# Optimization experiments

Hardware: AMD Instinct MI355X
Metric: run time of the kernel (lower is better)

Reference implementation:

```python
import jax, jax.numpy as jnp
import numpy as np
from jax import lax

B, C, H, W = 8, 512, 64, 64
HM, WM = 256, 256
EPS = 1e-08


def _nearest_downsample(mask, H_out, W_out):
    # torch F.interpolate(mode='nearest'): src_idx = floor(dst_idx * in/out)
    h_in, w_in = mask.shape[-2:]
    ri = (jnp.arange(H_out) * h_in) // H_out
    ci = (jnp.arange(W_out) * w_in) // W_out
    return mask[:, :, ri][:, :, :, ci]


def _dilate3x3(m):
    # binary dilation with 3x3 ones structuring element == 3x3 max-pool, zero pad
    return lax.reduce_window(m, 0.0, lax.max, (1, 1, 3, 3), (1, 1, 1, 1),
                             [(0, 0), (0, 0), (1, 1), (1, 1)])


def _edt(mask2d):
    # Exact Euclidean distance from each pixel to nearest mask==1 pixel.
    # mask2d: [B, H, W] float 0/1. Separable two-pass squared EDT.
    b, h, w = mask2d.shape
    BIG = jnp.asarray(h + w, mask2d.dtype)
    rows = jnp.arange(h)
    di = jnp.abs(rows[:, None] - rows[None, :]).astype(mask2d.dtype)  # [H, H']
    # g[b,i,j] = min_{i'} |i - i'| s.t. mask[b,i',j]==1 (BIG if column empty)
    g = jnp.min(di[None, :, :, None] + BIG * (1.0 - mask2d)[:, None, :, :], axis=2)  # [B,H,W]
    cols = jnp.arange(w)
    dj2 = ((cols[:, None] - cols[None, :]) ** 2).astype(mask2d.dtype)  # [W, W']
    d2 = jnp.min(g[:, :, None, :] ** 2 + dj2[None, None, :, :], axis=3)  # [B,H,W]
    dist = jnp.sqrt(d2)
    dist = dist / (jnp.max(dist, axis=(1, 2), keepdims=True) + 1e-06)
    return dist


def setup_inputs() -> dict:
    key = jax.random.key(0)
    k1, k2, k3, k4, k5 = jax.random.split(key, 5)
    f_s = jax.random.normal(k1, (B, C, H, W), dtype=jnp.float32)
    support_mask = jax.random.randint(k2, (B, 1, HM, WM), 0, 2, dtype=jnp.int32)
    sg = 1.0 / np.sqrt(C)
    gate_w = jax.random.uniform(k3, (C, C), jnp.float32, -sg, sg)
    gate_b = jnp.zeros((C,), jnp.float32)
    sf = 1.0 / np.sqrt(C + 1)
    fusion_w = jax.random.uniform(k4, (C, C + 1), jnp.float32, -sf, sf)
    fusion_b = jnp.zeros((C,), jnp.float32)
    return {"f_s": f_s, "support_mask": support_mask, "gate_w": gate_w,
            "gate_b": gate_b, "fusion_w": fusion_w, "fusion_b": fusion_b}


def reference(f_s, support_mask, gate_w, gate_b, fusion_w, fusion_b):
    m_s = _nearest_downsample(support_mask, f_s.shape[2], f_s.shape[3]).astype(f_s.dtype)  # [B,1,H,W]
    m_dil = _dilate3x3(m_s)
    m_bg = jnp.clip(m_dil - m_s, 0.0, None)

    p_fg = jnp.sum(f_s * m_s, axis=(2, 3)) / (jnp.sum(m_s, axis=(2, 3)) + EPS)   # [B,C]
    p_bg = jnp.sum(f_s * m_bg, axis=(2, 3)) / (jnp.sum(m_bg, axis=(2, 3)) + EPS)  # [B,C]
    p_contrast = (p_fg - p_bg)[:, :, None, None]

    gate = jax.nn.sigmoid(jnp.einsum('bchw,oc->bohw', f_s, gate_w) + gate_b[None, :, None, None])
    f_pur = f_s + gate * p_contrast

    dist = _edt(m_s[:, 0])[:, None]  # [B,1,H,W]
    x = jnp.concatenate([f_pur, dist], axis=1)  # [B,C+1,H,W]
    out = jnp.einsum('bchw,oc->bohw', x, fusion_w) + fusion_b[None, :, None, None]
    return jax.nn.relu(out)
```

## Files before the change

### kernel.cpp

```cpp
#include <hip/hip_runtime.h>
#include <math.h>

#define NB 8
#define CC 512
#define NPIX 4096
#define HM 256

#define WS_MS    0
#define WS_MBG   32768
#define WS_DIST  65536
#define WS_CNT   98304
#define WS_PC    98320
#define WS_GWP   102416
#define WS_FWP   364560
#define WS_FSPK  626704
#define WS_FPPK  17403920

typedef __attribute__((ext_vector_type(8))) short short8;
typedef __attribute__((ext_vector_type(4))) float f32x4;

__device__ __forceinline__ uint32_t packbf(float x) {
    uint32_t b = __float_as_uint(x);
    uint32_t hi = (b + 0x7fffu + ((b >> 16) & 1u)) & 0xffff0000u;
    float rem = x - __uint_as_float(hi);
    uint32_t rb = __float_as_uint(rem);
    uint32_t lo = (rb + 0x7fffu + ((rb >> 16) & 1u)) >> 16;
    return hi | lo;
}
__device__ __forceinline__ float unpackf(uint32_t u) {
    return __uint_as_float(u & 0xffff0000u) + __uint_as_float(u << 16);
}

__device__ __forceinline__ float wave_sum(float v) {
#pragma unroll
    for (int o = 32; o > 0; o >>= 1) v += __shfl_down(v, o, 64);
    return v;
}
__device__ __forceinline__ float wave_max(float v) {
#pragma unroll
    for (int o = 32; o > 0; o >>= 1) v = fmaxf(v, __shfl_down(v, o, 64));
    return v;
}

__global__ __launch_bounds__(1024) void mask_edt_kernel(
    const int* __restrict__ mask, float* __restrict__ ms, float* __restrict__ mbg,
    float* __restrict__ dist, float* __restrict__ cnt)
{
    __shared__ float sm[4096];
    __shared__ float sg[4096];
    __shared__ float red[32];

    const int b = blockIdx.x;
    const int t = threadIdx.x;
    const int wid = t >> 6, lane = t & 63;
    const int* mb = mask + b * (HM * HM);

#pragma unroll
    for (int u = 0; u < 4; ++u) {
        int p = u * 1024 + t;
        int i = p >> 6, j = p & 63;
        sm[p] = (float)mb[(i * 4) * HM + (j * 4)];
    }
    __syncthreads();

    float cfg = 0.f, cbg = 0.f;
#pragma unroll
    for (int u = 0; u < 4; ++u) {
        int p = u * 1024 + t;
        int i = p >> 6, j = p & 63;
        float mx = 0.f;
#pragma unroll
        for (int di = -1; di <= 1; ++di) {
            int ii = i + di;
            if (ii < 0 || ii > 63) continue;
#pragma unroll
            for (int dj = -1; dj <= 1; ++dj) {
                int jj = j + dj;
                if (jj < 0 || jj > 63) continue;
                mx = fmaxf(mx, sm[ii * 64 + jj]);
            }
        }
        float m = sm[p];
        float bg = fmaxf(mx - m, 0.f);
        cfg += m; cbg += bg;
        ms[b * NPIX + p] = m;
        mbg[b * NPIX + p] = bg;
    }
    float s1 = wave_sum(cfg), s2 = wave_sum(cbg);
    if (lane == 0) { red[wid] = s1; red[16 + wid] = s2; }
    __syncthreads();
    if (t == 0) {
        float a = 0.f, g = 0.f;
#pragma unroll
        for (int w = 0; w < 16; ++w) { a += red[w]; g += red[16 + w]; }
        cnt[b] = a; cnt[8 + b] = g;
    }

#pragma unroll 1
    for (int u = 0; u < 4; ++u) {
        int p = u * 1024 + t;
        int i = p >> 6, j = p & 63;
        float fi = (float)i;
        float best = 1e30f;
#pragma unroll 8
        for (int ii = 0; ii < 64; ++ii) {
            float v = fabsf(fi - (float)ii) + 128.f * (1.f - sm[ii * 64 + j]);
            best = fminf(best, v);
        }
        sg[p] = best;
    }
    __syncthreads();

    float dmx = 0.f;
#pragma unroll 1
    for (int u = 0; u < 4; ++u) {
        int p = u * 1024 + t;
        int i = p >> 6, j = p & 63;
        float fj = (float)j;
        float best = 1e30f;
#pragma unroll 8
        for (int jj = 0; jj < 64; ++jj) {
            float g = sg[i * 64 + jj];
            float dj = fj - (float)jj;
            best = fminf(best, fmaf(g, g, dj * dj));
        }
        float d = sqrtf(best);
        sm[p] = d;
        dmx = fmaxf(dmx, d);
    }
    __syncthreads();
    float mW = wave_max(dmx);
    if (lane == 0) red[wid] = mW;
    __syncthreads();
    float dmax = red[0];
#pragma unroll
    for (int w = 1; w < 16; ++w) dmax = fmaxf(dmax, red[w]);
    dmax += 1e-6f;
#pragma unroll
    for (int u = 0; u < 4; ++u) {
        int p = u * 1024 + t;
        dist[b * NPIX + p] = sm[p] / dmax;
    }
}

__global__ __launch_bounds__(256) void pcontrast_kernel(
    const float* __restrict__ F, const float* __restrict__ ms,
    const float* __restrict__ mbg, const float* __restrict__ cnt,
    float* __restrict__ pc)
{
    const int c = blockIdx.x, b = blockIdx.y, t = threadIdx.x;
    const float4* f4 = (const float4*)(F + ((size_t)b * CC + c) * NPIX);
    const float4* m4 = (const float4*)(ms + (size_t)b * NPIX);
    const float4* g4 = (const float4*)(mbg + (size_t)b * NPIX);
    float sfg = 0.f, sbg = 0.f;
#pragma unroll 4
    for (int idx = t; idx < NPIX / 4; idx += 256) {
        float4 v = f4[idx], m = m4[idx], g = g4[idx];
        sfg += v.x * m.x + v.y * m.y + v.z * m.z + v.w * m.w;
        sbg += v.x * g.x + v.y * g.y + v.z * g.z + v.w * g.w;
    }
    __shared__ float r1[4], r2[4];
    sfg = wave_sum(sfg); sbg = wave_sum(sbg);
    int wid = t >> 6, lane = t & 63;
    if (lane == 0) { r1[wid] = sfg; r2[wid] = sbg; }
    __syncthreads();
    if (t == 0) {
        float a = r1[0] + r1[1] + r1[2] + r1[3];
        float g = r2[0] + r2[1] + r2[2] + r2[3];
        pc[b * CC + c] = a / (cnt[b] + 1e-8f) - g / (cnt[8 + b] + 1e-8f);
    }
}

__global__ __launch_bounds__(256) void transpose_pack(
    const float* __restrict__ F, uint32_t* __restrict__ Fp)
{
    __shared__ float sm[64][65];
    const int b  = blockIdx.z;
    const int c0 = blockIdx.y * 64;
    const int p0 = blockIdx.x * 64;
    const int t  = threadIdx.x;
    const float* Fb = F + ((size_t)b * CC + c0) * NPIX + p0;
#pragma unroll
    for (int s = 0; s < 4; ++s) {
        int cl = s * 16 + (t >> 4);
        float4 v = *(const float4*)&Fb[(size_t)cl * NPIX + (t & 15) * 4];
        *(float4*)&sm[cl][(t & 15) * 4] = v;
    }
    __syncthreads();
    const int lane = t & 63, w = t >> 6;
    uint32_t* Op = Fp + ((size_t)b * NPIX + p0) * CC + c0;
#pragma unroll
    for (int s = 0; s < 16; ++s) {
        int pl = s * 4 + w;
        Op[(size_t)pl * CC + lane] = packbf(sm[lane][pl]);
    }
}

__global__ __launch_bounds__(256) void pack_weights(
    const float* __restrict__ gw, const float* __restrict__ fw,
    uint32_t* __restrict__ gwp, uint32_t* __restrict__ fwp)
{
    const int o = blockIdx.x, t = threadIdx.x;
#pragma unroll 2
    for (int c = t; c < CC; c += 256) {
        gwp[o * CC + c] = packbf(gw[o * CC + c]);
        fwp[o * CC + c] = packbf(fw[o * (CC + 1) + c]);
    }
}

#define STAGE_TILE(dA, dB, ktU)                                                          \
    do {                                                                                 \
        _Pragma("unroll")                                                                \
        for (int r_ = 0; r_ < 4; ++r_) {                                                 \
            int grp_ = r_ * 4 + wid;                                                     \
            int row_ = grp_ * 8 + l8;                                                    \
            const uint32_t* gA_ = Ab + (size_t)(mBase + row_) * CC + (ktU) + k16src * 4; \
            const uint32_t* gB_ = Bb + (size_t)(nBase + row_) * CC + (ktU) + k16src * 4; \
            __builtin_amdgcn_global_load_lds(                                            \
                (const __attribute__((address_space(1))) uint32_t*)gA_,                  \
                (__attribute__((address_space(3))) uint32_t*)&dA[grp_ * 256 + lane * 4], \
                16, 0, 0);                                                               \
            __builtin_amdgcn_global_load_lds(                                            \
                (const __attribute__((address_space(1))) uint32_t*)gB_,                  \
                (__attribute__((address_space(3))) uint32_t*)&dB[grp_ * 256 + lane * 4], \
                16, 0, 0);                                                               \
        }                                                                                \
    } while (0)

#define COMPUTE_TILE(sA, sB)                                                             \
    do {                                                                                 \
        short8 hA_[4], lA_[4];                                                           \
        _Pragma("unroll")                                                                \
        for (int fm_ = 0; fm_ < 4; ++fm_) {                                              \
            int row_ = wr * 64 + fm_ * 16 + fr;                                          \
            int base_ = row_ * 32, s_ = row_ & 7;                                        \
            uint4 x0_ = *(const uint4*)&sA[base_ + (((kc * 2)     ^ s_) << 2)];          \
            uint4 x1_ = *(const uint4*)&sA[base_ + (((kc * 2 + 1) ^ s_) << 2)];          \
            uint32_t pk_[8] = {x0_.x, x0_.y, x0_.z, x0_.w, x1_.x, x1_.y, x1_.z, x1_.w};  \
            _Pragma("unroll")                                                            \
            for (int j_ = 0; j_ < 8; ++j_) {                                             \
                hA_[fm_][j_] = (short)(pk_[j_] >> 16);                                   \
                lA_[fm_][j_] = (short)(pk_[j_] & 0xffffu);                               \
            }                                                                            \
        }                                                                                \
        _Pragma("unroll")                                                                \
        for (int fn_ = 0; fn_ < 4; ++fn_) {                                              \
            int row_ = wc * 64 + fn_ * 16 + fr;                                          \
            int base_ = row_ * 32, s_ = row_ & 7;                                        \
            uint4 x0_ = *(const uint4*)&sB[base_ + (((kc * 2)     ^ s_) << 2)];          \
            uint4 x1_ = *(const uint4*)&sB[base_ + (((kc * 2 + 1) ^ s_) << 2)];          \
            uint32_t pk_[8] = {x0_.x, x0_.y, x0_.z, x0_.w, x1_.x, x1_.y, x1_.z, x1_.w};  \
            short8 hB_, lB_;                                                             \
            _Pragma("unroll")                                                            \
            for (int j_ = 0; j_ < 8; ++j_) {                                             \
                hB_[j_] = (short)(pk_[j_] >> 16);                                        \
                lB_[j_] = (short)(pk_[j_] & 0xffffu);                                    \
            }                                                                            \
            _Pragma("unroll")                                                            \
            for (int fm_ = 0; fm_ < 4; ++fm_) {                                          \
                acc[fm_][fn_] = __builtin_amdgcn_mfma_f32_16x16x32_bf16(hA_[fm_], hB_, acc[fm_][fn_], 0, 0, 0); \
                acc[fm_][fn_] = __builtin_amdgcn_mfma_f32_16x16x32_bf16(hA_[fm_], lB_, acc[fm_][fn_], 0, 0, 0); \
                acc[fm_][fn_] = __builtin_amdgcn_mfma_f32_16x16x32_bf16(lA_[fm_], hB_, acc[fm_][fn_], 0, 0, 0); \
            }                                                                            \
        }                                                                                \
    } while (0)

template <int MODE>
__global__ __launch_bounds__(256, 2) void mfma_gemm(
    const uint32_t* __restrict__ Apk, const uint32_t* __restrict__ Bpk,
    long aStride, long bStride,
    const float* __restrict__ bias,
    const float* __restrict__ aux,
    const float* __restrict__ wsrc,
    void* __restrict__ outp)
{
    const int gx = gridDim.x, gy = gridDim.y;
    const int nwg = gx * gy * gridDim.z;
    int lin = (blockIdx.z * gy + blockIdx.y) * gx + blockIdx.x;
    int cpx = nwg >> 3;
    int swz = (lin & 7) * cpx + (lin >> 3);
    const int bx = swz % gx;
    const int by = (swz / gx) % gy;
    const int b  = swz / (gx * gy);

    const int nBase = bx * 128;
    const int mBase = by * 128;
    const int tid   = threadIdx.x;
    const int lane  = tid & 63, wid = tid >> 6;
    const int wr    = wid >> 1, wc = wid & 1;

    __shared__ uint32_t As0[128 * 32];
    __shared__ uint32_t Bs0[128 * 32];
    __shared__ uint32_t As1[128 * 32];
    __shared__ uint32_t Bs1[128 * 32];

    const uint32_t* Ab = Apk + (size_t)b * aStride;
    const uint32_t* Bb = Bpk + (size_t)b * bStride;

    f32x4 acc[4][4];
#pragma unroll
    for (int i = 0; i < 4; ++i)
#pragma unroll
        for (int j = 0; j < 4; ++j) acc[i][j] = (f32x4){0.f, 0.f, 0.f, 0.f};

    const int l8 = lane >> 3;
    const int k16src = (lane & 7) ^ l8;
    const int fr = lane & 15;
    const int kc = lane >> 4;

    STAGE_TILE(As0, Bs0, 0);
    __syncthreads();

#pragma unroll 1
    for (int it2 = 0; it2 < 8; ++it2) {
        const int ktU1 = it2 * 64 + 32;
        STAGE_TILE(As1, Bs1, ktU1);
        COMPUTE_TILE(As0, Bs0);
        __syncthreads();
        if (it2 < 7) {
            STAGE_TILE(As0, Bs0, ktU1 + 32);
        }
        COMPUTE_TILE(As1, Bs1);
        __syncthreads();
    }

    const int rrow = (lane >> 4) * 4;
    if constexpr (MODE == 0) {
        uint32_t* fpur = (uint32_t*)outp;
#pragma unroll
        for (int fn = 0; fn < 4; ++fn) {
            int o = nBase + wc * 64 + fn * 16 + fr;
            float bo  = bias[o];
            float pco = aux[(size_t)b * CC + o];
#pragma unroll
            for (int fm = 0; fm < 4; ++fm) {
#pragma unroll
                for (int r = 0; r < 4; ++r) {
                    int p = mBase + wr * 64 + fm * 16 + rrow + r;
                    size_t idx = (size_t)p * CC + o;
                    float fs = unpackf(Ab[idx]);
                    float z = acc[fm][fn][r] + bo;
                    float g = 1.f / (1.f + expf(-z));
                    fpur[(size_t)b * NPIX * CC + idx] = packbf(fs + g * pco);
                }
            }
        }
    } else {
        float* Out = (float*)outp;
#pragma unroll
        for (int fn = 0; fn < 4; ++fn) {
            int p = nBase + wc * 64 + fn * 16 + fr;
            float dv = aux[(size_t)b * NPIX + p];
#pragma unroll
            for (int fm = 0; fm < 4; ++fm) {
#pragma unroll
                for (int r = 0; r < 4; ++r) {
                    int o = mBase + wr * 64 + fm * 16 + rrow + r;
                    float z = acc[fm][fn][r] + bias[o] + wsrc[(size_t)o * (CC + 1) + CC] * dv;
                    Out[((size_t)b * CC + o) * NPIX + p] = fmaxf(z, 0.f);
                }
            }
        }
    }
}

extern "C" void kernel_launch(void* const* d_in, const int* in_sizes, int n_in,
                              void* d_out, int out_size, void* d_ws, size_t ws_size,
                              hipStream_t stream)
{
    const float* f_s      = (const float*)d_in[0];
    const int*   mask     = (const int*)d_in[1];
    const float* gate_w   = (const float*)d_in[2];
    const float* gate_b   = (const float*)d_in[3];
    const float* fusion_w = (const float*)d_in[4];
    const float* fusion_b = (const float*)d_in[5];
    float* out = (float*)d_out;
    float*    wsf = (float*)d_ws;
    uint32_t* wsu = (uint32_t*)d_ws;

    float* ms   = wsf + WS_MS;
    float* mbg  = wsf + WS_MBG;
    float* dist = wsf + WS_DIST;
    float* cnt  = wsf + WS_CNT;
    float* pc   = wsf + WS_PC;
    uint32_t* gwp  = wsu + WS_GWP;
    uint32_t* fwp  = wsu + WS_FWP;
    uint32_t* fspk = wsu + WS_FSPK;
    uint32_t* fppk = wsu + WS_FPPK;

    hipLaunchKernelGGL(mask_edt_kernel, dim3(NB), dim3(1024), 0, stream,
                       mask, ms, mbg, dist, cnt);
    hipLaunchKernelGGL(pack_weights, dim3(CC), dim3(256), 0, stream,
                       gate_w, fusion_w, gwp, fwp);
    hipLaunchKernelGGL(transpose_pack, dim3(NPIX / 64, CC / 64, NB), dim3(256), 0, stream,
                       f_s, fspk);
    hipLaunchKernelGGL(pcontrast_kernel, dim3(CC, NB), dim3(256), 0, stream,
                       f_s, ms, mbg, cnt, pc);
    hipLaunchKernelGGL((mfma_gemm<0>), dim3(CC / 128, NPIX / 128, NB), dim3(256), 0, stream,
                       fspk, gwp, (long)NPIX * CC, 0L, gate_b, pc, (const float*)nullptr,
                       (void*)fppk);
    hipLaunchKernelGGL((mfma_gemm<1>), dim3(NPIX / 128, CC / 128, NB), dim3(256), 0, stream,
                       fwp, fppk, 0L, (long)NPIX * CC, fusion_b, dist, fusion_w,
                       (void*)out);
}
```

Measured before the change: 344.5 us.

## Store split-bf16 operands as separate hi and lo planes instead of packed words

Each fp32 value is still split into a high and a low bf16 half. These halves are now written by the pack, transpose and gate-GEMM epilogue kernels into two separate ushort arrays instead of one packed uint32 array. The GEMM stages four planes into LDS and loads short8 fragments directly, removing the per-element shift and mask unpacking before each MFMA. In exchange it drops the XOR swizzle, which may cause LDS bank conflicts. It also doubles the number of narrower 2-byte scattered loads and stores in the epilogue.

```diff
diff --git a/kernel.cpp b/kernel.cpp
--- a/kernel.cpp
+++ b/kernel.cpp
@@ -11,10 +11,14 @@
 #define WS_DIST  65536
 #define WS_CNT   98304
 #define WS_PC    98320
-#define WS_GWP   102416
-#define WS_FWP   364560
-#define WS_FSPK  626704
-#define WS_FPPK  17403920
+#define WS_GWH   102416
+#define WS_GWL   233488
+#define WS_FWH   364560
+#define WS_FWL   495632
+#define WS_FSH   626704
+#define WS_FSL   9015312
+#define WS_FPH   17403920
+#define WS_FPL   25792528
 
 typedef __attribute__((ext_vector_type(8))) short short8;
 typedef __attribute__((ext_vector_type(4))) float f32x4;
@@ -27,8 +31,8 @@
     uint32_t lo = (rb + 0x7fffu + ((rb >> 16) & 1u)) >> 16;
     return hi | lo;
 }
-__device__ __forceinline__ float unpackf(uint32_t u) {
-    return __uint_as_float(u & 0xffff0000u) + __uint_as_float(u << 16);
+__device__ __forceinline__ float joinbf(uint32_t h, uint32_t l) {
+    return __uint_as_float(h << 16) + __uint_as_float(l << 16);
 }
 
 __device__ __forceinline__ float wave_sum(float v) {
@@ -172,7 +176,7 @@
 }
 
 __global__ __launch_bounds__(256) void transpose_pack(
-    const float* __restrict__ F, uint32_t* __restrict__ Fp)
+    const float* __restrict__ F, ushort* __restrict__ Fh, ushort* __restrict__ Fl)
 {
     __shared__ float sm[64][65];
     const int b  = blockIdx.z;
@@ -188,74 +192,67 @@
     }
     __syncthreads();
     const int lane = t & 63, w = t >> 6;
-    uint32_t* Op = Fp + ((size_t)b * NPIX + p0) * CC + c0;
+    size_t ob = ((size_t)b * NPIX + p0) * CC + c0;
 #pragma unroll
     for (int s = 0; s < 16; ++s) {
         int pl = s * 4 + w;
-        Op[(size_t)pl * CC + lane] = packbf(sm[lane][pl]);
+        uint32_t u = packbf(sm[lane][pl]);
+        Fh[ob + (size_t)pl * CC + lane] = (ushort)(u >> 16);
+        Fl[ob + (size_t)pl * CC + lane] = (ushort)(u & 0xffffu);
     }
 }
 
 __global__ __launch_bounds__(256) void pack_weights(
     const float* __restrict__ gw, const float* __restrict__ fw,
-    uint32_t* __restrict__ gwp, uint32_t* __restrict__ fwp)
+    ushort* __restrict__ gwh, ushort* __restrict__ gwl,
+    ushort* __restrict__ fwh, ushort* __restrict__ fwl)
 {
     const int o = blockIdx.x, t = threadIdx.x;
 #pragma unroll 2
     for (int c = t; c < CC; c += 256) {
-        gwp[o * CC + c] = packbf(gw[o * CC + c]);
-        fwp[o * CC + c] = packbf(fw[o * (CC + 1) + c]);
-    }
-}
-
-#define STAGE_TILE(dA, dB, ktU)                                                          \
+        uint32_t ug = packbf(gw[o * CC + c]);
+        uint32_t uf = packbf(fw[o * (CC + 1) + c]);
+        gwh[o * CC + c] = (ushort)(ug >> 16); gwl[o * CC + c] = (ushort)(ug & 0xffffu);
+        fwh[o * CC + c] = (ushort)(uf >> 16); fwl[o * CC + c] = (ushort)(uf & 0xffffu);
+    }
+}
+
+#define STAGE_PLANE(dst, gsrc)                                                           \
     do {                                                                                 \
         _Pragma("unroll")                                                                \
-        for (int r_ = 0; r_ < 4; ++r_) {                                                 \
-            int grp_ = r_ * 4 + wid;                                                     \
-            int row_ = grp_ * 8 + l8;                                                    \
-            const uint32_t* gA_ = Ab + (size_t)(mBase + row_) * CC + (ktU) + k16src * 4; \
-            const uint32_t* gB_ = Bb + (size_t)(nBase + row_) * CC + (ktU) + k16src * 4; \
+        for (int c_ = 0; c_ < 2; ++c_) {                                                 \
+            int grp_ = c_ * 4 + wid;                                                     \
+            const ushort* s_ = (gsrc) + (size_t)(grp_ * 16 + (lane >> 2)) * CC           \
+                               + (lane & 3) * 8;                                         \
             __builtin_amdgcn_global_load_lds(                                            \
-                (const __attribute__((address_space(1))) uint32_t*)gA_,                  \
-                (__attribute__((address_space(3))) uint32_t*)&dA[grp_ * 256 + lane * 4], \
-                16, 0, 0);                                                               \
-            __builtin_amdgcn_global_load_lds(                                            \
-                (const __attribute__((address_space(1))) uint32_t*)gB_,                  \
-                (__attribute__((address_space(3))) uint32_t*)&dB[grp_ * 256 + lane * 4], \
+                (const __attribute__((address_space(1))) uint32_t*)s_,                   \
+                (__attribute__((address_space(3))) uint32_t*)&dst[grp_ * 256 + lane * 4],\
                 16, 0, 0);                                                               \
         }                                                                                \
     } while (0)
 
-#define COMPUTE_TILE(sA, sB)                                                             \
+#define STAGE_TILE(dAh, dAl, dBh, dBl, ktE)                                              \
+    do {                                                                                 \
+        STAGE_PLANE(dAh, Abh + (size_t)mBase * CC + (ktE));                              \
+        STAGE_PLANE(dAl, Abl + (size_t)mBase * CC + (ktE));                              \
+        STAGE_PLANE(dBh, Bbh + (size_t)nBase * CC + (ktE));                              \
+        STAGE_PLANE(dBl, Bbl + (size_t)nBase * CC + (ktE));                              \
+    } while (0)
+
+#define COMPUTE_TILE(sAh, sAl, sBh, sBl)                                                 \
     do {                                                                                 \
         short8 hA_[4], lA_[4];                                                           \
         _Pragma("unroll")                                                                \
         for (int fm_ = 0; fm_ < 4; ++fm_) {                                              \
-            int row_ = wr * 64 + fm_ * 16 + fr;                                          \
-            int base_ = row_ * 32, s_ = row_ & 7;                                        \
-            uint4 x0_ = *(const uint4*)&sA[base_ + (((kc * 2)     ^ s_) << 2)];          \
-            uint4 x1_ = *(const uint4*)&sA[base_ + (((kc * 2 + 1) ^ s_) << 2)];          \
-            uint32_t pk_[8] = {x0_.x, x0_.y, x0_.z, x0_.w, x1_.x, x1_.y, x1_.z, x1_.w};  \
-            _Pragma("unroll")                                                            \
-            for (int j_ = 0; j_ < 8; ++j_) {                                             \
-                hA_[fm_][j_] = (short)(pk_[j_] >> 16);                                   \
-                lA_[fm_][j_] = (short)(pk_[j_] & 0xffffu);                               \
-            }                                                                            \
+            int ro_ = (wr * 64 + fm_ * 16 + fr) * 32 + kc * 8;         \
+            hA_[fm_] = *(const short8*)((const ushort*)sAh + ro_);                       \
+            lA_[fm_] = *(const short8*)((const ushort*)sAl + ro_);                       \
         }                                                                                \
         _Pragma("unroll")                                                                \
         for (int fn_ = 0; fn_ < 4; ++fn_) {                                              \
-            int row_ = wc * 64 + fn_ * 16 + fr;                                          \
-            int base_ = row_ * 32, s_ = row_ & 7;                                        \
-            uint4 x0_ = *(const uint4*)&sB[base_ + (((kc * 2)     ^ s_) << 2)];          \
-            uint4 x1_ = *(const uint4*)&sB[base_ + (((kc * 2 + 1) ^ s_) << 2)];          \
-            uint32_t pk_[8] = {x0_.x, x0_.y, x0_.z, x0_.w, x1_.x, x1_.y, x1_.z, x1_.w};  \
-            short8 hB_, lB_;                                                             \
-            _Pragma("unroll")                                                            \
-            for (int j_ = 0; j_ < 8; ++j_) {                                             \
-                hB_[j_] = (short)(pk_[j_] >> 16);                                        \
-                lB_[j_] = (short)(pk_[j_] & 0xffffu);                                    \
-            }                                                                            \
+            int ro_ = (wc * 64 + fn_ * 16 + fr) * 32 + kc * 8;                           \
+            short8 hB_ = *(const short8*)((const ushort*)sBh + ro_);                     \
+            short8 lB_ = *(const short8*)((const ushort*)sBl + ro_);                     \
             _Pragma("unroll")                                                            \
             for (int fm_ = 0; fm_ < 4; ++fm_) {                                          \
                 acc[fm_][fn_] = __builtin_amdgcn_mfma_f32_16x16x32_bf16(hA_[fm_], hB_, acc[fm_][fn_], 0, 0, 0); \
@@ -267,12 +264,15 @@
 
 template <int MODE>
 __global__ __launch_bounds__(256, 2) void mfma_gemm(
-    const uint32_t* __restrict__ Apk, const uint32_t* __restrict__ Bpk,
+    const ushort* __restrict__ Aph, const ushort* __restrict__ Apl,
+    const ushort* __restrict__ Bph, const ushort* __restrict__ Bpl,
     long aStride, long bStride,
     const float* __restrict__ bias,
     const float* __restrict__ aux,
     const float* __restrict__ wsrc,
-    void* __restrict__ outp)
+    ushort* __restrict__ oh,
+    ushort* __restrict__ ol,
+    float* __restrict__ of)
 {
     const int gx = gridDim.x, gy = gridDim.y;
     const int nwg = gx * gy * gridDim.z;
@@ -289,13 +289,13 @@
     const int lane  = tid & 63, wid = tid >> 6;
     const int wr    = wid >> 1, wc = wid & 1;
 
-    __shared__ uint32_t As0[128 * 32];
-    __shared__ uint32_t Bs0[128 * 32];
-    __shared__ uint32_t As1[128 * 32];
-    __shared__ uint32_t Bs1[128 * 32];
-
-    const uint32_t* Ab = Apk + (size_t)b * aStride;
-    const uint32_t* Bb = Bpk + (size_t)b * bStride;
+    __shared__ uint32_t Ah0[2048], Al0[2048], Bh0[2048], Bl0[2048];
+    __shared__ uint32_t Ah1[2048], Al1[2048], Bh1[2048], Bl1[2048];
+
+    const ushort* Abh = Aph + (size_t)b * aStride;
+    const ushort* Abl = Apl + (size_t)b * aStride;
+    const ushort* Bbh = Bph + (size_t)b * bStride;
+    const ushort* Bbl = Bpl + (size_t)b * bStride;
 
     f32x4 acc[4][4];
 #pragma unroll
@@ -303,30 +303,27 @@
 #pragma unroll
         for (int j = 0; j < 4; ++j) acc[i][j] = (f32x4){0.f, 0.f, 0.f, 0.f};
 
-    const int l8 = lane >> 3;
-    const int k16src = (lane & 7) ^ l8;
     const int fr = lane & 15;
     const int kc = lane >> 4;
 
-    STAGE_TILE(As0, Bs0, 0);
+    STAGE_TILE(Ah0, Al0, Bh0, Bl0, 0);
     __syncthreads();
 
 #pragma unroll 1
     for (int it2 = 0; it2 < 8; ++it2) {
-        const int ktU1 = it2 * 64 + 32;
-        STAGE_TILE(As1, Bs1, ktU1);
-        COMPUTE_TILE(As0, Bs0);
+        const int ktE1 = it2 * 64 + 32;
+        STAGE_TILE(Ah1, Al1, Bh1, Bl1, ktE1);
+        COMPUTE_TILE(Ah0, Al0, Bh0, Bl0);
         __syncthreads();
         if (it2 < 7) {
-            STAGE_TILE(As0, Bs0, ktU1 + 32);
-        }
-        COMPUTE_TILE(As1, Bs1);
+            STAGE_TILE(Ah0, Al0, Bh0, Bl0, ktE1 + 32);
+        }
+        COMPUTE_TILE(Ah1, Al1, Bh1, Bl1);
         __syncthreads();
     }
 
     const int rrow = (lane >> 4) * 4;
     if constexpr (MODE == 0) {
-        uint32_t* fpur = (uint32_t*)outp;
 #pragma unroll
         for (int fn = 0; fn < 4; ++fn) {
             int o = nBase + wc * 64 + fn * 16 + fr;
@@ -338,15 +335,17 @@
                 for (int r = 0; r < 4; ++r) {
                     int p = mBase + wr * 64 + fm * 16 + rrow + r;
                     size_t idx = (size_t)p * CC + o;
-                    float fs = unpackf(Ab[idx]);
+                    float fs = joinbf(Abh[idx], Abl[idx]);
                     float z = acc[fm][fn][r] + bo;
                     float g = 1.f / (1.f + expf(-z));
-                    fpur[(size_t)b * NPIX * CC + idx] = packbf(fs + g * pco);
+                    uint32_t u = packbf(fs + g * pco);
+                    size_t gidx = (size_t)b * NPIX * CC + idx;
+                    oh[gidx] = (ushort)(u >> 16);
+                    ol[gidx] = (ushort)(u & 0xffffu);
                 }
             }
         }
     } else {
-        float* Out = (float*)outp;
 #pragma unroll
         for (int fn = 0; fn < 4; ++fn) {
             int p = nBase + wc * 64 + fn * 16 + fr;
@@ -357,7 +356,7 @@
                 for (int r = 0; r < 4; ++r) {
                     int o = mBase + wr * 64 + fm * 16 + rrow + r;
                     float z = acc[fm][fn][r] + bias[o] + wsrc[(size_t)o * (CC + 1) + CC] * dv;
-                    Out[((size_t)b * CC + o) * NPIX + p] = fmaxf(z, 0.f);
+                    of[((size_t)b * CC + o) * NPIX + p] = fmaxf(z, 0.f);
                 }
             }
         }
@@ -375,7 +374,7 @@
     const float* fusion_w = (const float*)d_in[4];
     const float* fusion_b = (const float*)d_in[5];
     float* out = (float*)d_out;
-    float*    wsf = (float*)d_ws;
+    float*  wsf = (float*)d_ws;
     uint32_t* wsu = (uint32_t*)d_ws;
 
     float* ms   = wsf + WS_MS;
@@ -383,23 +382,27 @@
     float* dist = wsf + WS_DIST;
     float* cnt  = wsf + WS_CNT;
     float* pc   = wsf + WS_PC;
-    uint32_t* gwp  = wsu + WS_GWP;
-    uint32_t* fwp  = wsu + WS_FWP;
-    uint32_t* fspk = wsu + WS_FSPK;
-    uint32_t* fppk = wsu + WS_FPPK;
+    ushort* gwh = (ushort*)(wsu + WS_GWH);
+    ushort* gwl = (ushort*)(wsu + WS_GWL);
+    ushort* fwh = (ushort*)(wsu + WS_FWH);
+    ushort* fwl = (ushort*)(wsu + WS_FWL);
+    ushort* fsh = (ushort*)(wsu + WS_FSH);
+    ushort* fsl = (ushort*)(wsu + WS_FSL);
+    ushort* fph = (ushort*)(wsu + WS_FPH);
+    ushort* fpl = (ushort*)(wsu + WS_FPL);
 
     hipLaunchKernelGGL(mask_edt_kernel, dim3(NB), dim3(1024), 0, stream,
                        mask, ms, mbg, dist, cnt);
     hipLaunchKernelGGL(pack_weights, dim3(CC), dim3(256), 0, stream,
-                       gate_w, fusion_w, gwp, fwp);
+                       gate_w, fusion_w, gwh, gwl, fwh, fwl);
     hipLaunchKernelGGL(transpose_pack, dim3(NPIX / 64, CC / 64, NB), dim3(256), 0, stream,
-                       f_s, fspk);
+                       f_s, fsh, fsl);
     hipLaunchKernelGGL(pcontrast_kernel, dim3(CC, NB), dim3(256), 0, stream,
                        f_s, ms, mbg, cnt, pc);
     hipLaunchKernelGGL((mfma_gemm<0>), dim3(CC / 128, NPIX / 128, NB), dim3(256), 0, stream,
-                       fspk, gwp, (long)NPIX * CC, 0L, gate_b, pc, (const float*)nullptr,
-                       (void*)fppk);
+                       fsh, fsl, gwh, gwl, (long)NPIX * CC, 0L, gate_b, pc,
+                       (const float*)nullptr, fph, fpl, (float*)nullptr);
     hipLaunchKernelGGL((mfma_gemm<1>), dim3(NPIX / 128, CC / 128, NB), dim3(256), 0, stream,
-                       fwp, fppk, 0L, (long)NPIX * CC, fusion_b, dist, fusion_w,
-                       (void*)out);
-}
+                       fwh, fwl, fph, fpl, 0L, (long)NPIX * CC, fusion_b, dist,
+                       fusion_w, (ushort*)nullptr, (ushort*)nullptr, out);
+}
```

After: 350.4 us. No clear change (+1.7%).
